# Kernel tuning notes

Hardware: AMD Instinct MI355X
Metric: run time of the kernel (lower is better)

The kernel has to match this reference:

```python
import jax, jax.numpy as jnp
import numpy as np

NUM_HEADS = 64
HEAD_DIM = 64
HIDDEN = 2048
STATE = 128
GROUPS = 1
CONVK = 4
CHUNK = 256
INTER = 2 * HIDDEN                       # expand * hidden_size = 4096
CONV_DIM = INTER + 2 * GROUPS * STATE    # 4352
PROJ = INTER + CONV_DIM + NUM_HEADS      # 8512
EPS = 1e-5


def segment_sum(x):
    # x: (..., T) -> (..., T, T) with out[i,j] = sum_{j<k<=i} x[k], -inf above diag
    T = x.shape[-1]
    xe = jnp.broadcast_to(x[..., None], x.shape + (T,))  # [..., i, j] = x[..., i]
    mask_lo = jnp.tril(jnp.ones((T, T), bool), -1)
    xe = jnp.where(mask_lo, xe, 0.0)
    cs = jnp.cumsum(xe, axis=-2)
    mask = jnp.tril(jnp.ones((T, T), bool), 0)
    return jnp.where(mask, cs, -jnp.inf)


def setup_inputs() -> dict:
    key = jax.random.key(0)
    ks = jax.random.split(key, 8)
    b, l = 2, 2048
    s = 0.02
    return {
        "hidden_states": jax.random.normal(ks[0], (b, l, HIDDEN), jnp.float32),
        "in_proj_w": jax.random.normal(ks[1], (PROJ, HIDDEN), jnp.float32) * s,
        "in_proj_b": jax.random.normal(ks[2], (PROJ,), jnp.float32) * 0.01,
        "conv_w": jax.random.normal(ks[3], (CONV_DIM, CONVK), jnp.float32) * 0.1,  # depthwise kernel (torch weight[:,0,:])
        "dt_bias": jnp.ones((NUM_HEADS,), jnp.float32),
        "A_log": jnp.log(jnp.arange(1, NUM_HEADS + 1, dtype=jnp.float32)),
        "D": jnp.ones((NUM_HEADS,), jnp.float32),
        "norm_w": jnp.ones((INTER,), jnp.float32),
        "out_proj_w": jax.random.normal(ks[4], (HIDDEN, INTER), jnp.float32) * s,
        "out_proj_b": jnp.zeros((HIDDEN,), jnp.float32),
    }


def reference(hidden_states, in_proj_w, in_proj_b, conv_w, dt_bias, A_log, D,
              norm_w, out_proj_w, out_proj_b):
    b, l, _ = hidden_states.shape
    proj = hidden_states @ in_proj_w.T + in_proj_b            # (b,l,PROJ)
    gate, hbc, dt = jnp.split(proj, [INTER, INTER + CONV_DIM], axis=-1)

    # causal depthwise conv1d (padding=K-1, truncated to seq_len) + SiLU
    xp = jnp.pad(hbc, ((0, 0), (CONVK - 1, 0), (0, 0)))
    conv = sum(xp[:, j:j + l, :] * conv_w[:, j] for j in range(CONVK))
    hbc = jax.nn.silu(conv)

    x, B, C = jnp.split(hbc, [INTER, INTER + GROUPS * STATE], axis=-1)
    A = -jnp.exp(A_log)                                       # (h,)
    dt = jax.nn.softplus(dt + dt_bias)                        # (b,l,h)
    dt = jnp.clip(dt, 0.0, None)                              # time_step_limit = (0, inf)

    x = x.reshape(b, l, NUM_HEADS, HEAD_DIM)                  # (b,l,h,p)
    rep = NUM_HEADS // GROUPS
    Bh = jnp.repeat(B.reshape(b, l, GROUPS, STATE), rep, axis=2)  # (b,l,h,n)
    Ch = jnp.repeat(C.reshape(b, l, GROUPS, STATE), rep, axis=2)

    pad = (CHUNK - l % CHUNK) % CHUNK

    def chunk(t):
        t = jnp.pad(t, ((0, 0), (0, pad)) + ((0, 0),) * (t.ndim - 2))
        return t.reshape(b, -1, CHUNK, *t.shape[2:])

    xc = chunk(x * dt[..., None])                             # (b,c,s,h,p) discretized x
    Ac = chunk(A * dt)                                        # (b,c,s,h)
    Bc = chunk(Bh)                                            # (b,c,s,h,n)
    Cc = chunk(Ch)

    Ach = jnp.transpose(Ac, (0, 3, 1, 2))                     # (b,h,c,s)
    A_cumsum = jnp.cumsum(Ach, axis=-1)

    # 1. intra-chunk (diagonal block) outputs
    L = jnp.exp(segment_sum(Ach))                             # (b,h,c,s,s)
    Y_diag = jnp.einsum('bcthn,bcshn,bhcts,bcshp->bcthp', Cc, Bc, L, xc)

    # 2. per-chunk final states
    decay_states = jnp.exp(A_cumsum[..., -1:] - A_cumsum)     # (b,h,c,s)
    states = jnp.einsum('bcshn,bhcs,bcshp->bchpn', Bc, decay_states, xc)

    # 3. inter-chunk recurrence
    A_last = jnp.pad(A_cumsum[..., -1], ((0, 0), (0, 0), (1, 0)))  # (b,h,c+1)
    decay_chunk = jnp.exp(segment_sum(A_last))                # (b,h,c+1,c+1)
    states0 = jnp.concatenate([jnp.zeros_like(states[:, :1]), states], axis=1)
    prev = jnp.einsum('bhzc,bchpn->bzhpn', decay_chunk, states0)[:, :-1]  # (b,c,h,p,n)

    # 4. state -> output contribution
    state_decay_out = jnp.exp(A_cumsum)                       # (b,h,c,s)
    Y_off = jnp.einsum('bcshn,bchpn,bhcs->bcshp', Cc, prev, state_decay_out)

    Y = (Y_diag + Y_off).reshape(b, -1, NUM_HEADS, HEAD_DIM)[:, :l]
    y = Y + D[:, None] * x                                    # D skip connection
    y = y.reshape(b, l, INTER)

    # gated RMSNorm (gate applied before normalization)
    g = y * jax.nn.silu(gate)
    var = jnp.mean(g * g, axis=-1, keepdims=True)
    g = g * jax.lax.rsqrt(var + EPS) * norm_w

    return g @ out_proj_w.T + out_proj_b                      # (b,l,HIDDEN)
```

## Files before the change

### kernel.cpp

```cpp
#include <hip/hip_runtime.h>

typedef __bf16 bf16;
typedef __bf16 bf16x8 __attribute__((ext_vector_type(8)));
typedef __bf16 bf16x4 __attribute__((ext_vector_type(4)));
typedef float  floatx4 __attribute__((ext_vector_type(4)));

#define HIDDEN   2048
#define NUMH     64
#define HDIM     64
#define STATE    128
#define INTER    4096
#define CONV_DIM 4352
#define PROJ_N   8512
#define PROJ_PAD 8576
#define SEQ      2048
#define BATCH    2
#define CHUNK    256
#define NCHUNK   8
#define ROWS     4096
#define DT_COL0  8448

#define GLDS(gp, lp) __builtin_amdgcn_global_load_lds(                      \
    (const __attribute__((address_space(1))) void*)(gp),                    \
    (__attribute__((address_space(3))) void*)(lp), 16, 0, 0)

__global__ __launch_bounds__(256) void cvt_bf16_kernel(
    const float* __restrict__ in, bf16* __restrict__ out, long n, long srcn) {
  long i = ((long)blockIdx.x * 256 + threadIdx.x) * 4;
  if (i >= n) return;
  if (i + 3 < srcn) {
    const float* p = in + i;
    bf16x4 o;
    o[0] = (bf16)p[0]; o[1] = (bf16)p[1]; o[2] = (bf16)p[2]; o[3] = (bf16)p[3];
    *(bf16x4*)(out + i) = o;
  } else {
    for (int j = 0; j < 4; j++) {
      float v = (i + j < srcn) ? in[i + j] : 0.f;
      out[i + j] = (bf16)v;
    }
  }
}

__global__ __launch_bounds__(256, 2) void gemm_bt_kernel(
    const bf16* __restrict__ A, const bf16* __restrict__ B,
    const float* __restrict__ bias, bf16* __restrict__ Cb,
    float* __restrict__ Cf, float* __restrict__ ds,
    int M, int N, int K, int bias_n, int dt0) {
  __shared__ __align__(16) bf16 lA[2 * 128 * 32];
  __shared__ __align__(16) bf16 lB[2 * 128 * 32];
  const int tid  = threadIdx.x;
  const int lane = tid & 63;
  const int wave = tid >> 6;
  const int gm = M >> 7;
  const int id = blockIdx.x;
  const int xcd = id & 7;
  const int j = id >> 3;
  const int mstripe = gm >> 3;
  const int mb = xcd * mstripe + (j % mstripe);
  const int nb = j / mstripe;
  const int m0 = mb * 128;
  const int n0 = nb * 128;
  const int wm = (wave >> 1) * 64;
  const int wn = (wave & 1) * 64;
  const int q  = lane >> 4;
  const int ln = lane & 15;
  const int r0 = tid >> 2;
  const int c0 = (tid & 3) * 8;

  floatx4 acc[4][4] = {};

  const bf16* Ap = A + (long)(m0 + r0) * K + c0;
  const bf16* Bp = B + (long)(n0 + r0) * K + c0;
  bf16* lAw = lA + wave * 512;
  bf16* lBw = lB + wave * 512;

  for (int k0 = 0; k0 < K; k0 += 64) {
    __syncthreads();
    GLDS(Ap + k0, lAw);
    GLDS(Ap + (long)64 * K + k0, lAw + 2048);
    GLDS(Ap + k0 + 32, lAw + 4096);
    GLDS(Ap + (long)64 * K + k0 + 32, lAw + 6144);
    GLDS(Bp + k0, lBw);
    GLDS(Bp + (long)64 * K + k0, lBw + 2048);
    GLDS(Bp + k0 + 32, lBw + 4096);
    GLDS(Bp + (long)64 * K + k0 + 32, lBw + 6144);
    __syncthreads();
#pragma unroll
    for (int kc = 0; kc < 2; kc++) {
      bf16x8 af[4], bg[4];
#pragma unroll
      for (int i = 0; i < 4; i++) {
        af[i] = *(const bf16x8*)(lA + kc * 4096 + (wm + i * 16 + ln) * 32 + q * 8);
        bg[i] = *(const bf16x8*)(lB + kc * 4096 + (wn + i * 16 + ln) * 32 + q * 8);
      }
#pragma unroll
      for (int mi = 0; mi < 4; mi++)
#pragma unroll
        for (int ni = 0; ni < 4; ni++)
          acc[mi][ni] = __builtin_amdgcn_mfma_f32_16x16x32_bf16(
              af[mi], bg[ni], acc[mi][ni], 0, 0, 0);
    }
  }

#pragma unroll
  for (int mi = 0; mi < 4; mi++) {
#pragma unroll
    for (int ni = 0; ni < 4; ni++) {
      int col = n0 + wn + ni * 16 + ln;
      float bv = (col < bias_n) ? bias[col] : 0.f;
#pragma unroll
      for (int r = 0; r < 4; r++) {
        int row = m0 + wm + mi * 16 + q * 4 + r;
        float v = acc[mi][ni][r] + bv;
        if (Cb) Cb[(long)row * N + col] = (bf16)v;
        else    Cf[(long)row * N + col] = v;
        if (ds && col >= dt0 && col < dt0 + 64)
          ds[(long)row * 64 + (col - dt0)] = v;
      }
    }
  }
}

__global__ __launch_bounds__(256) void conv_silu_kernel(
    const bf16* __restrict__ proj, const float* __restrict__ cw,
    bf16* __restrict__ out) {
  long i = ((long)blockIdx.x * 256 + threadIdx.x) * 4;
  if (i >= (long)ROWS * CONV_DIM) return;
  int ch = (int)(i % CONV_DIM);
  long bl = i / CONV_DIM;
  int l = (int)(bl & (SEQ - 1));
  const bf16* p = proj + bl * PROJ_PAD + INTER + ch;
  float a[4] = {0.f, 0.f, 0.f, 0.f};
#pragma unroll
  for (int tap = 0; tap < 4; tap++) {
    int back = 3 - tap;
    if (l >= back) {
      bf16x4 v = *(const bf16x4*)(p - (long)back * PROJ_PAD);
#pragma unroll
      for (int j = 0; j < 4; j++) a[j] += (float)v[j] * cw[(ch + j) * 4 + tap];
    }
  }
  bf16x4 o;
#pragma unroll
  for (int j = 0; j < 4; j++) {
    float s = a[j] / (1.f + expf(-a[j]));
    o[j] = (bf16)s;
  }
  *(bf16x4*)(out + i) = o;
}

__global__ __launch_bounds__(256) void dt_scan_kernel(
    const float* __restrict__ dtraw, const float* __restrict__ dt_bias,
    const float* __restrict__ A_log, float* __restrict__ dtb,
    float* __restrict__ cumA) {
  int idx = blockIdx.x;
  int c = idx & 7, h = (idx >> 3) & 63, b = idx >> 9;
  int s = threadIdx.x;
  long row = (long)b * SEQ + c * CHUNK + s;
  float x = dtraw[row * NUMH + h] + dt_bias[h];
  float dt = (x > 20.f) ? x : log1pf(expf(x));
  dtb[row * NUMH + h] = dt;
  float dA = -expf(A_log[h]) * dt;
  __shared__ float sc[256];
  sc[s] = dA;
  __syncthreads();
  for (int off = 1; off < 256; off <<= 1) {
    float v = (s >= off) ? sc[s - off] : 0.f;
    __syncthreads();
    sc[s] += v;
    __syncthreads();
  }
  cumA[(long)idx * 256 + s] = sc[s];
}

__global__ __launch_bounds__(256, 2) void g_kernel(
    const bf16* __restrict__ conv, float* __restrict__ G) {
  int bc = blockIdx.x, tt = blockIdx.y, sb = blockIdx.z;
  if (sb > tt) return;
  int b = bc >> 3, c = bc & 7;
  int tid = threadIdx.x, lane = tid & 63, w = tid >> 6;
  int q = lane >> 4, ln = lane & 15;
  __shared__ __align__(16) bf16 sCg[4 * 64 * 32];
  __shared__ __align__(16) bf16 sBg[4 * 64 * 32];
  long rowBase = (long)b * SEQ + c * CHUNK;
  for (int i = tid; i < 1024; i += 256) {
    int r = i >> 4, n0 = (i & 15) * 8;
    int base = ((n0 >> 5) * 64 + r) * 32 + (n0 & 31);
    bf16x8 cv = *(const bf16x8*)(conv + (rowBase + tt * 64 + r) * CONV_DIM + INTER + STATE + n0);
    *(bf16x8*)(sCg + base) = cv;
    bf16x8 bv = *(const bf16x8*)(conv + (rowBase + sb * 64 + r) * CONV_DIM + INTER + n0);
    *(bf16x8*)(sBg + base) = bv;
  }
  __syncthreads();
  floatx4 acc[4] = {};
#pragma unroll
  for (int kc = 0; kc < 4; kc++) {
    bf16x8 af = *(const bf16x8*)(sCg + (kc * 64 + w * 16 + ln) * 32 + q * 8);
#pragma unroll
    for (int ni = 0; ni < 4; ni++) {
      bf16x8 bg = *(const bf16x8*)(sBg + (kc * 64 + ni * 16 + ln) * 32 + q * 8);
      acc[ni] = __builtin_amdgcn_mfma_f32_16x16x32_bf16(af, bg, acc[ni], 0, 0, 0);
    }
  }
  float* Gb = G + ((long)bc << 16);
#pragma unroll
  for (int ni = 0; ni < 4; ni++) {
    int s = sb * 64 + ni * 16 + ln;
#pragma unroll
    for (int r = 0; r < 4; r++) {
      int t = tt * 64 + w * 16 + q * 4 + r;
      Gb[(long)t * 256 + s] = acc[ni][r];
    }
  }
}

__global__ __launch_bounds__(256, 2) void states_kernel(
    const bf16* __restrict__ conv, const float* __restrict__ dtb,
    const float* __restrict__ cumA, float* __restrict__ S) {
  int idx = blockIdx.x;
  int h = idx & 63, c = (idx >> 6) & 7, b = idx >> 9;
  int tid = threadIdx.x, lane = tid & 63, w = tid >> 6;
  int q = lane >> 4, ln = lane & 15;
  __shared__ __align__(16) bf16 sBT[2 * 128 * 32];
  __shared__ __align__(16) bf16 sXT[2 * 64 * 32];
  long caBase = ((long)(b * 64 + h) * 8 + c) * 256;
  float aLast = cumA[caBase + 255];
  long rowBase = (long)b * SEQ + c * CHUNK;
  floatx4 acc[2][4] = {};
  for (int s0 = 0; s0 < 256; s0 += 64) {
    __syncthreads();
    for (int i = tid; i < 1024; i += 256) {
      int sl = i >> 4, n0 = (i & 15) * 8;
      bf16x8 v = *(const bf16x8*)(conv + (rowBase + s0 + sl) * CONV_DIM + INTER + n0);
      int base = ((sl >> 5) * 128 + n0) * 32 + (sl & 31);
#pragma unroll
      for (int jj = 0; jj < 8; jj++) sBT[base + jj * 32] = v[jj];
    }
    for (int i = tid; i < 512; i += 256) {
      int sl = i >> 3, p0 = (i & 7) * 8;
      long row = rowBase + s0 + sl;
      float wgt = __expf(aLast - cumA[caBase + s0 + sl]) * dtb[row * NUMH + h];
      bf16x8 v = *(const bf16x8*)(conv + row * CONV_DIM + h * HDIM + p0);
      int base = ((sl >> 5) * 64 + p0) * 32 + (sl & 31);
#pragma unroll
      for (int jj = 0; jj < 8; jj++) sXT[base + jj * 32] = (bf16)((float)v[jj] * wgt);
    }
    __syncthreads();
#pragma unroll
    for (int kc = 0; kc < 2; kc++) {
      bf16x8 af[2], bg[4];
#pragma unroll
      for (int mi = 0; mi < 2; mi++)
        af[mi] = *(const bf16x8*)(sBT + (kc * 128 + w * 32 + mi * 16 + ln) * 32 + q * 8);
#pragma unroll
      for (int ni = 0; ni < 4; ni++)
        bg[ni] = *(const bf16x8*)(sXT + (kc * 64 + ni * 16 + ln) * 32 + q * 8);
#pragma unroll
      for (int mi = 0; mi < 2; mi++)
#pragma unroll
        for (int ni = 0; ni < 4; ni++)
          acc[mi][ni] = __builtin_amdgcn_mfma_f32_16x16x32_bf16(
              af[mi], bg[ni], acc[mi][ni], 0, 0, 0);
    }
  }
  float* Sp = S + ((long)idx << 13);
#pragma unroll
  for (int mi = 0; mi < 2; mi++)
#pragma unroll
    for (int ni = 0; ni < 4; ni++) {
      int p = ni * 16 + ln;
#pragma unroll
      for (int r = 0; r < 4; r++) {
        int n = w * 32 + mi * 16 + q * 4 + r;
        Sp[n * 64 + p] = acc[mi][ni][r];
      }
    }
}

__global__ __launch_bounds__(256) void recur_kernel(
    const float* __restrict__ S, const float* __restrict__ cumA,
    float* __restrict__ P) {
  int bh = blockIdx.x, kq = blockIdx.y;
  int b = bh >> 6, h = bh & 63;
  int tid = threadIdx.x;
  float p[8];
#pragma unroll
  for (int k = 0; k < 8; k++) p[k] = 0.f;
  for (int c = 0; c < 8; c++) {
    long blk = ((long)(b * 8 + c) * 64 + h) << 13;
#pragma unroll
    for (int k = 0; k < 8; k++) P[blk + (kq * 8 + k) * 256 + tid] = p[k];
    float e = __expf(cumA[((long)bh * 8 + c) * 256 + 255]);
#pragma unroll
    for (int k = 0; k < 8; k++) p[k] = S[blk + (kq * 8 + k) * 256 + tid] + e * p[k];
  }
}

__global__ __launch_bounds__(256, 2) void y_kernel(
    const bf16* __restrict__ conv, const float* __restrict__ dtb,
    const float* __restrict__ cumA, const float* __restrict__ G,
    const float* __restrict__ P, const float* __restrict__ D,
    bf16* __restrict__ ybuf) {
  int idx = blockIdx.x;
  int h = idx & 63, c = (idx >> 6) & 7, b = idx >> 9;
  int tid = threadIdx.x, lane = tid & 63, w = tid >> 6;
  int q = lane >> 4, ln = lane & 15;
  __shared__ __align__(16) bf16 sPT[128 * 64];
  __shared__ __align__(16) bf16 sXT[256 * 64];
  __shared__ float scA[256];
  __shared__ float sE[256];
  long caBase = ((long)(b * 64 + h) * 8 + c) * 256;
  long rowBase = (long)b * SEQ + c * CHUNK;
  const float* Gbase = G + ((long)(b * 8 + c) << 16);

  float myA = cumA[caBase + tid];
  scA[tid] = myA;
  {
    const float* Pblk = P + ((long)idx << 13);
    int n = tid >> 1;
    int p0 = (tid & 1) * 32;
    int nc = (n >> 5) * 64, nk = n & 31;
#pragma unroll
    for (int pp = 0; pp < 32; pp += 4) {
      floatx4 v = *(const floatx4*)(Pblk + n * 64 + p0 + pp);
#pragma unroll
      for (int j = 0; j < 4; j++)
        sPT[(nc + p0 + pp + j) * 32 + nk] = (bf16)v[j];
    }
  }
  {
    int s = tid;
    long row = rowBase + s;
    float dt = dtb[row * NUMH + h];
    int sc = (s >> 5) * 64, sk = s & 31;
    const bf16* xr = conv + row * CONV_DIM + h * HDIM;
#pragma unroll
    for (int p0 = 0; p0 < 64; p0 += 8) {
      bf16x8 xv = *(const bf16x8*)(xr + p0);
#pragma unroll
      for (int j = 0; j < 8; j++)
        sXT[(sc + p0 + j) * 32 + sk] = (bf16)((float)xv[j] * dt);
    }
  }
  __syncthreads();
  sE[tid] = __expf(scA[tid | 63] - myA);

  floatx4 acc[4][4] = {};

  const bf16* Cbase = conv + (rowBase + w * 64) * CONV_DIM + INTER + STATE;
  for (int k0 = 0; k0 < 128; k0 += 32) {
    bf16x8 af[4], bg[4];
#pragma unroll
    for (int mi = 0; mi < 4; mi++)
      af[mi] = *(const bf16x8*)(Cbase + (long)(mi * 16 + ln) * CONV_DIM + k0 + q * 8);
#pragma unroll
    for (int ni = 0; ni < 4; ni++)
      bg[ni] = *(const bf16x8*)(sPT + ((k0 >> 5) * 64 + ni * 16 + ln) * 32 + q * 8);
#pragma unroll
    for (int mi = 0; mi < 4; mi++)
#pragma unroll
      for (int ni = 0; ni < 4; ni++)
        acc[mi][ni] = __builtin_amdgcn_mfma_f32_16x16x32_bf16(
            af[mi], bg[ni], acc[mi][ni], 0, 0, 0);
  }
#pragma unroll
  for (int mi = 0; mi < 4; mi++)
#pragma unroll
    for (int r = 0; r < 4; r++) {
      float e = __expf(scA[w * 64 + mi * 16 + q * 4 + r]);
#pragma unroll
      for (int ni = 0; ni < 4; ni++) acc[mi][ni][r] *= e;
    }
  __syncthreads();

  for (int sb = 0; sb < w; sb++) {
    float Rm[4];
#pragma unroll
    for (int mi = 0; mi < 4; mi++)
      Rm[mi] = __expf(scA[w * 64 + mi * 16 + ln] - scA[sb * 64 + 63]);
#pragma unroll
    for (int kk = 0; kk < 64; kk += 32) {
      int s0 = sb * 64 + kk;
      bf16x8 af[4], bg[4];
#pragma unroll
      for (int mi = 0; mi < 4; mi++) {
        int t = w * 64 + mi * 16 + ln;
        const float* Gr = Gbase + (long)t * 256 + s0 + q * 8;
        floatx4 g0 = *(const floatx4*)Gr;
        floatx4 g1 = *(const floatx4*)(Gr + 4);
        bf16x8 m;
#pragma unroll
        for (int j = 0; j < 4; j++)
          m[j] = (bf16)(g0[j] * Rm[mi] * sE[s0 + q * 8 + j]);
#pragma unroll
        for (int j = 4; j < 8; j++)
          m[j] = (bf16)(g1[j - 4] * Rm[mi] * sE[s0 + q * 8 + j]);
        af[mi] = m;
      }
#pragma unroll
      for (int ni = 0; ni < 4; ni++)
        bg[ni] = *(const bf16x8*)(sXT + ((s0 >> 5) * 64 + ni * 16 + ln) * 32 + q * 8);
#pragma unroll
      for (int mi = 0; mi < 4; mi++)
#pragma unroll
        for (int ni = 0; ni < 4; ni++)
          acc[mi][ni] = __builtin_amdgcn_mfma_f32_16x16x32_bf16(
              af[mi], bg[ni], acc[mi][ni], 0, 0, 0);
    }
  }

  {
    int sb = w;
#pragma unroll
    for (int kk = 0; kk < 64; kk += 32) {
      int s0 = sb * 64 + kk;
      bf16x8 af[4], bg[4];
#pragma unroll
      for (int mi = 0; mi < 4; mi++) {
        int t = w * 64 + mi * 16 + ln;
        float cAt = scA[t];
        const float* Gr = Gbase + (long)t * 256 + s0 + q * 8;
        floatx4 g0 = *(const floatx4*)Gr;
        floatx4 g1 = *(const floatx4*)(Gr + 4);
        bf16x8 m;
#pragma unroll
        for (int j = 0; j < 4; j++) {
          int s = s0 + q * 8 + j;
          float v = g0[j] * __expf(cAt - scA[s]);
          m[j] = (bf16)((s <= t) ? v : 0.f);
        }
#pragma unroll
        for (int j = 4; j < 8; j++) {
          int s = s0 + q * 8 + j;
          float v = g1[j - 4] * __expf(cAt - scA[s]);
          m[j] = (bf16)((s <= t) ? v : 0.f);
        }
        af[mi] = m;
      }
#pragma unroll
      for (int ni = 0; ni < 4; ni++)
        bg[ni] = *(const bf16x8*)(sXT + ((s0 >> 5) * 64 + ni * 16 + ln) * 32 + q * 8);
#pragma unroll
      for (int mi = 0; mi < 4; mi++)
#pragma unroll
        for (int ni = 0; ni < 4; ni++)
          acc[mi][ni] = __builtin_amdgcn_mfma_f32_16x16x32_bf16(
              af[mi], bg[ni], acc[mi][ni], 0, 0, 0);
    }
  }

  float d = D[h];
#pragma unroll
  for (int mi = 0; mi < 4; mi++)
#pragma unroll
    for (int ni = 0; ni < 4; ni++) {
      int col = ni * 16 + ln;
#pragma unroll
      for (int r = 0; r < 4; r++) {
        long row = rowBase + w * 64 + mi * 16 + q * 4 + r;
        float xv = (float)conv[row * CONV_DIM + h * HDIM + col];
        ybuf[row * INTER + h * HDIM + col] = (bf16)(acc[mi][ni][r] + d * xv);
      }
    }
}

__global__ __launch_bounds__(256) void rmsnorm_kernel(
    const bf16* __restrict__ ybuf, const bf16* __restrict__ proj,
    const float* __restrict__ nw, bf16* __restrict__ gb) {
  long row = blockIdx.x;
  int tid = threadIdx.x;
  float gv[16];
  float ss = 0.f;
#pragma unroll
  for (int k = 0; k < 16; k++) {
    int i = k * 256 + tid;
    float y = (float)ybuf[row * INTER + i];
    float gt = (float)proj[row * PROJ_PAD + i];
    float g = y * (gt / (1.f + expf(-gt)));
    gv[k] = g;
    ss += g * g;
  }
#pragma unroll
  for (int off = 32; off > 0; off >>= 1) ss += __shfl_down(ss, off, 64);
  __shared__ float red[4];
  if ((tid & 63) == 0) red[tid >> 6] = ss;
  __syncthreads();
  float tot = red[0] + red[1] + red[2] + red[3];
  float scale = rsqrtf(tot * (1.f / 4096.f) + 1e-5f);
#pragma unroll
  for (int k = 0; k < 16; k++) {
    int i = k * 256 + tid;
    gb[row * INTER + i] = (bf16)(gv[k] * scale * nw[i]);
  }
}

extern "C" void kernel_launch(void* const* d_in, const int* in_sizes, int n_in,
                              void* d_out, int out_size, void* d_ws, size_t ws_size,
                              hipStream_t stream) {
  const float* hs   = (const float*)d_in[0];
  const float* ipw  = (const float*)d_in[1];
  const float* ipb  = (const float*)d_in[2];
  const float* cw   = (const float*)d_in[3];
  const float* dtbi = (const float*)d_in[4];
  const float* alog = (const float*)d_in[5];
  const float* Dp   = (const float*)d_in[6];
  const float* nw   = (const float*)d_in[7];
  const float* opw  = (const float*)d_in[8];
  const float* opb  = (const float*)d_in[9];
  float* out = (float*)d_out;

  char* ws = (char*)d_ws;
  bf16*  hsb   = (bf16*)(ws + 0);
  bf16*  wb    = (bf16*)(ws + 16777216);
  float* S     = (float*)(ws + 0);
  bf16*  ybuf  = (bf16*)(ws + 0);
  bf16*  owb   = (bf16*)(ws + 35127296);
  bf16*  proj  = (bf16*)(ws + 51904512);
  bf16*  conv  = (bf16*)(ws + 122159104);
  float* dtraw = (float*)(ws + 157810688);
  float* dtb   = (float*)(ws + 158859264);
  float* cumA  = (float*)(ws + 159907840);
  float* G     = (float*)(ws + 160956416);
  float* P     = (float*)(ws + 165150720);
  bf16*  gb    = (bf16*)(ws + 165150720);

  cvt_bf16_kernel<<<8192, 256, 0, stream>>>(hs, hsb, (long)ROWS * HIDDEN, (long)ROWS * HIDDEN);
  cvt_bf16_kernel<<<17152, 256, 0, stream>>>(ipw, wb, (long)PROJ_PAD * HIDDEN, (long)PROJ_N * HIDDEN);

  gemm_bt_kernel<<<(PROJ_PAD / 128) * (ROWS / 128), 256, 0, stream>>>(
      hsb, wb, ipb, proj, nullptr, dtraw, ROWS, PROJ_PAD, HIDDEN, PROJ_N, DT_COL0);

  cvt_bf16_kernel<<<8192, 256, 0, stream>>>(opw, owb, (long)HIDDEN * INTER, (long)HIDDEN * INTER);

  conv_silu_kernel<<<17408, 256, 0, stream>>>(proj, cw, conv);

  dt_scan_kernel<<<1024, 256, 0, stream>>>(dtraw, dtbi, alog, dtb, cumA);

  g_kernel<<<dim3(16, 4, 4), 256, 0, stream>>>(conv, G);

  states_kernel<<<1024, 256, 0, stream>>>(conv, dtb, cumA, S);

  recur_kernel<<<dim3(128, 4), 256, 0, stream>>>(S, cumA, P);

  y_kernel<<<1024, 256, 0, stream>>>(conv, dtb, cumA, G, P, Dp, ybuf);

  rmsnorm_kernel<<<4096, 256, 0, stream>>>(ybuf, proj, nw, gb);

  gemm_bt_kernel<<<(HIDDEN / 128) * (ROWS / 128), 256, 0, stream>>>(
      gb, owb, opb, nullptr, out, nullptr, ROWS, HIDDEN, INTER, HIDDEN, 1 << 30);
}
```

Baseline: 662.0 us.

## Use 256x256-tile double-buffered GEMM kernel for input projection

Adds a new 512-thread GEMM kernel with 256x256 output tiles, swizzled LDS, direct global-to-LDS loads, double buffering and MFMA scheduling hints, and uses it for the input projection. The projection width is padded to 8704 so it divides by 256, and the workspace offsets are shifted to match. Larger tiles raise arithmetic intensity and cut redundant global loads, but padding adds wasted columns and fewer, bigger blocks may hurt occupancy or tail balance.

```diff
diff --git a/kernel.cpp b/kernel.cpp
--- a/kernel.cpp
+++ b/kernel.cpp
@@ -12,7 +12,7 @@
 #define INTER    4096
 #define CONV_DIM 4352
 #define PROJ_N   8512
-#define PROJ_PAD 8576
+#define PROJ_PAD 8704
 #define SEQ      2048
 #define BATCH    2
 #define CHUNK    256
@@ -37,6 +37,127 @@
     for (int j = 0; j < 4; j++) {
       float v = (i + j < srcn) ? in[i + j] : 0.f;
       out[i + j] = (bf16)v;
+    }
+  }
+}
+
+__global__ __launch_bounds__(512, 4) void gemm256_kernel(
+    const bf16* __restrict__ A, const bf16* __restrict__ B,
+    const float* __restrict__ bias, bf16* __restrict__ Cb,
+    float* __restrict__ ds,
+    int M, int N, int K, int bias_n, int dt0) {
+  __shared__ __align__(16) bf16 lA0[256 * 32], lA1[256 * 32];
+  __shared__ __align__(16) bf16 lB0[256 * 32], lB1[256 * 32];
+  const int tid  = threadIdx.x;
+  const int lane = tid & 63;
+  const int wave = tid >> 6;
+  const int wm   = wave >> 2;
+  const int wn   = wave & 3;
+  const int q    = lane >> 4;
+  const int ln   = lane & 15;
+
+  const int mtiles  = M >> 8;
+  const int mstripe = mtiles >> 3;
+  const int id  = blockIdx.x;
+  const int xcd = id & 7;
+  const int jj  = id >> 3;
+  const int mb  = xcd * mstripe + (jj % mstripe);
+  const int nb  = jj / mstripe;
+  const int m0  = mb << 8;
+  const int n0  = nb << 8;
+
+  const int rA0 = tid >> 2;
+  const int rA1 = 128 + (tid >> 2);
+  const int cc  = tid & 3;
+  const int qa0 = cc ^ ((rA0 >> 1) & 3);
+  const int qa1 = cc ^ ((rA1 >> 1) & 3);
+  const bf16* srcA0 = A + (long)(m0 + rA0) * K + qa0 * 8;
+  const bf16* srcA1 = A + (long)(m0 + rA1) * K + qa1 * 8;
+  const bf16* srcB0 = B + (long)(n0 + rA0) * K + qa0 * 8;
+  const bf16* srcB1 = B + (long)(n0 + rA1) * K + qa1 * 8;
+
+  int aoff[8], boff[4];
+#pragma unroll
+  for (int mi = 0; mi < 8; mi++) {
+    int ra = wm * 128 + mi * 16 + ln;
+    aoff[mi] = ra * 32 + ((q ^ ((ra >> 1) & 3)) * 8);
+  }
+#pragma unroll
+  for (int ni = 0; ni < 4; ni++) {
+    int rb = wn * 64 + ni * 16 + ln;
+    boff[ni] = rb * 32 + ((q ^ ((rb >> 1) & 3)) * 8);
+  }
+
+  floatx4 acc[8][4] = {};
+
+  auto phase = [&](const bf16* aS, const bf16* bS, bf16* aD, bf16* bD,
+                   int kn, bool doStage) {
+    if (doStage) {
+      GLDS(srcA0 + kn, aD + wave * 512);
+      GLDS(srcA1 + kn, aD + 4096 + wave * 512);
+      GLDS(srcB0 + kn, bD + wave * 512);
+      GLDS(srcB1 + kn, bD + 4096 + wave * 512);
+    }
+    __builtin_amdgcn_sched_barrier(0);
+    bf16x8 af[8], bg[4];
+#pragma unroll
+    for (int mi = 0; mi < 4; mi++) af[mi] = *(const bf16x8*)(aS + aoff[mi]);
+#pragma unroll
+    for (int ni = 0; ni < 4; ni++) bg[ni] = *(const bf16x8*)(bS + boff[ni]);
+    __builtin_amdgcn_sched_barrier(0);
+#pragma unroll
+    for (int mi = 4; mi < 8; mi++) af[mi] = *(const bf16x8*)(aS + aoff[mi]);
+    asm volatile("s_waitcnt lgkmcnt(4)" ::: "memory");
+    __builtin_amdgcn_sched_barrier(0);
+    __builtin_amdgcn_s_setprio(1);
+#pragma unroll
+    for (int mi = 0; mi < 4; mi++)
+#pragma unroll
+      for (int ni = 0; ni < 4; ni++)
+        acc[mi][ni] = __builtin_amdgcn_mfma_f32_16x16x32_bf16(
+            af[mi], bg[ni], acc[mi][ni], 0, 0, 0);
+    __builtin_amdgcn_s_setprio(0);
+    asm volatile("s_waitcnt lgkmcnt(0)" ::: "memory");
+    __builtin_amdgcn_sched_barrier(0);
+    __builtin_amdgcn_s_setprio(1);
+#pragma unroll
+    for (int mi = 4; mi < 8; mi++)
+#pragma unroll
+      for (int ni = 0; ni < 4; ni++)
+        acc[mi][ni] = __builtin_amdgcn_mfma_f32_16x16x32_bf16(
+            af[mi], bg[ni], acc[mi][ni], 0, 0, 0);
+    __builtin_amdgcn_s_setprio(0);
+    asm volatile("s_waitcnt vmcnt(0)" ::: "memory");
+    __builtin_amdgcn_s_barrier();
+  };
+
+  GLDS(srcA0, lA0 + wave * 512);
+  GLDS(srcA1, lA0 + 4096 + wave * 512);
+  GLDS(srcB0, lB0 + wave * 512);
+  GLDS(srcB1, lB0 + 4096 + wave * 512);
+  asm volatile("s_waitcnt vmcnt(0)" ::: "memory");
+  __builtin_amdgcn_s_barrier();
+
+  const int NC = K >> 5;
+  for (int j = 0; j < NC; j += 2) {
+    phase(lA0, lB0, lA1, lB1, (j + 1) << 5, true);
+    phase(lA1, lB1, lA0, lB0, (j + 2) << 5, (j + 2) < NC);
+  }
+
+#pragma unroll
+  for (int mi = 0; mi < 8; mi++) {
+#pragma unroll
+    for (int ni = 0; ni < 4; ni++) {
+      int col = n0 + wn * 64 + ni * 16 + ln;
+      float bv = (col < bias_n) ? bias[col] : 0.f;
+#pragma unroll
+      for (int r = 0; r < 4; r++) {
+        int row = m0 + wm * 128 + mi * 16 + q * 4 + r;
+        float v = acc[mi][ni][r] + bv;
+        Cb[(long)row * N + col] = (bf16)v;
+        if (ds && col >= dt0 && col < dt0 + 64)
+          ds[(long)row * 64 + (col - dt0)] = v;
+      }
     }
   }
 }
@@ -515,20 +636,20 @@
   float* S     = (float*)(ws + 0);
   bf16*  ybuf  = (bf16*)(ws + 0);
   bf16*  owb   = (bf16*)(ws + 35127296);
-  bf16*  proj  = (bf16*)(ws + 51904512);
-  bf16*  conv  = (bf16*)(ws + 122159104);
-  float* dtraw = (float*)(ws + 157810688);
-  float* dtb   = (float*)(ws + 158859264);
-  float* cumA  = (float*)(ws + 159907840);
-  float* G     = (float*)(ws + 160956416);
-  float* P     = (float*)(ws + 165150720);
-  bf16*  gb    = (bf16*)(ws + 165150720);
+  bf16*  proj  = (bf16*)(ws + 52428800);
+  bf16*  conv  = (bf16*)(ws + 123731968);
+  float* dtraw = (float*)(ws + 159383552);
+  float* dtb   = (float*)(ws + 160432128);
+  float* cumA  = (float*)(ws + 161480704);
+  float* G     = (float*)(ws + 162529280);
+  float* P     = (float*)(ws + 166723584);
+  bf16*  gb    = (bf16*)(ws + 166723584);
 
   cvt_bf16_kernel<<<8192, 256, 0, stream>>>(hs, hsb, (long)ROWS * HIDDEN, (long)ROWS * HIDDEN);
-  cvt_bf16_kernel<<<17152, 256, 0, stream>>>(ipw, wb, (long)PROJ_PAD * HIDDEN, (long)PROJ_N * HIDDEN);
-
-  gemm_bt_kernel<<<(PROJ_PAD / 128) * (ROWS / 128), 256, 0, stream>>>(
-      hsb, wb, ipb, proj, nullptr, dtraw, ROWS, PROJ_PAD, HIDDEN, PROJ_N, DT_COL0);
+  cvt_bf16_kernel<<<17408, 256, 0, stream>>>(ipw, wb, (long)PROJ_PAD * HIDDEN, (long)PROJ_N * HIDDEN);
+
+  gemm256_kernel<<<(ROWS / 256) * (PROJ_PAD / 256), 512, 0, stream>>>(
+      hsb, wb, ipb, proj, dtraw, ROWS, PROJ_PAD, HIDDEN, PROJ_N, DT_COL0);
 
   cvt_bf16_kernel<<<8192, 256, 0, stream>>>(opw, owb, (long)HIDDEN * INTER, (long)HIDDEN * INTER);
 
```

Result: slower. 2.309 ms (+248.8%).

## Triple-buffer GEMM LDS tiles with swizzled layout and overlapped global loads

Applied to the files above, without the earlier changes.

Replaces the single-buffer, two-barrier-per-step GEMM mainloop with a three-stage LDS ring over K-steps of 32. The next tile is issued via global_load_lds while the current one is computed, with vmcnt-based waits and one barrier per step. It also XOR-swizzles the LDS column chunks to cut bank conflicts, and raises the MFMA priority during compute. Occupancy hint goes from 2 to 3 blocks per CU, which may raise register pressure, and there is more synchronization per unit of K.

```diff
diff --git a/kernel.cpp b/kernel.cpp
--- a/kernel.cpp
+++ b/kernel.cpp
@@ -41,13 +41,12 @@
   }
 }
 
-__global__ __launch_bounds__(256, 2) void gemm_bt_kernel(
+__global__ __launch_bounds__(256, 3) void gemm_bt_kernel(
     const bf16* __restrict__ A, const bf16* __restrict__ B,
     const float* __restrict__ bias, bf16* __restrict__ Cb,
     float* __restrict__ Cf, float* __restrict__ ds,
     int M, int N, int K, int bias_n, int dt0) {
-  __shared__ __align__(16) bf16 lA[2 * 128 * 32];
-  __shared__ __align__(16) bf16 lB[2 * 128 * 32];
+  __shared__ __align__(16) bf16 lds[3 * 8192];
   const int tid  = threadIdx.x;
   const int lane = tid & 63;
   const int wave = tid >> 6;
@@ -65,42 +64,82 @@
   const int q  = lane >> 4;
   const int ln = lane & 15;
   const int r0 = tid >> 2;
-  const int c0 = (tid & 3) * 8;
+  const int c0 = tid & 3;
+  const int qa = c0 ^ ((r0 >> 1) & 3);
+
+  const bf16* srcA = A + (long)(m0 + r0) * K + qa * 8;
+  const bf16* srcB = B + (long)(n0 + r0) * K + qa * 8;
+  const long rs64 = (long)64 * K;
+
+  int aoff[4], boff[4];
+#pragma unroll
+  for (int i = 0; i < 4; i++) {
+    int ra = wm + i * 16 + ln;
+    aoff[i] = ra * 32 + ((q ^ ((ra >> 1) & 3)) * 8);
+    int rb = wn + i * 16 + ln;
+    boff[i] = rb * 32 + ((q ^ ((rb >> 1) & 3)) * 8) + 4096;
+  }
 
   floatx4 acc[4][4] = {};
 
-  const bf16* Ap = A + (long)(m0 + r0) * K + c0;
-  const bf16* Bp = B + (long)(n0 + r0) * K + c0;
-  bf16* lAw = lA + wave * 512;
-  bf16* lBw = lB + wave * 512;
-
-  for (int k0 = 0; k0 < K; k0 += 64) {
-    __syncthreads();
-    GLDS(Ap + k0, lAw);
-    GLDS(Ap + (long)64 * K + k0, lAw + 2048);
-    GLDS(Ap + k0 + 32, lAw + 4096);
-    GLDS(Ap + (long)64 * K + k0 + 32, lAw + 6144);
-    GLDS(Bp + k0, lBw);
-    GLDS(Bp + (long)64 * K + k0, lBw + 2048);
-    GLDS(Bp + k0 + 32, lBw + 4096);
-    GLDS(Bp + (long)64 * K + k0 + 32, lBw + 6144);
-    __syncthreads();
-#pragma unroll
-    for (int kc = 0; kc < 2; kc++) {
-      bf16x8 af[4], bg[4];
-#pragma unroll
-      for (int i = 0; i < 4; i++) {
-        af[i] = *(const bf16x8*)(lA + kc * 4096 + (wm + i * 16 + ln) * 32 + q * 8);
-        bg[i] = *(const bf16x8*)(lB + kc * 4096 + (wn + i * 16 + ln) * 32 + q * 8);
-      }
-#pragma unroll
-      for (int mi = 0; mi < 4; mi++)
-#pragma unroll
-        for (int ni = 0; ni < 4; ni++)
-          acc[mi][ni] = __builtin_amdgcn_mfma_f32_16x16x32_bf16(
-              af[mi], bg[ni], acc[mi][ni], 0, 0, 0);
-    }
-  }
+#define STAGE(gA, gB, so)                                                   \
+  do {                                                                      \
+    bf16* dA = lds + (so) + wave * 512;                                     \
+    bf16* dB = lds + (so) + 4096 + wave * 512;                              \
+    GLDS((gA), dA);                                                         \
+    GLDS((gA) + rs64, dA + 2048);                                           \
+    GLDS((gB), dB);                                                         \
+    GLDS((gB) + rs64, dB + 2048);                                           \
+  } while (0)
+
+#define COMPUTE(so)                                                         \
+  do {                                                                      \
+    bf16x8 af[4], bg[4];                                                    \
+    _Pragma("unroll")                                                       \
+    for (int i = 0; i < 4; i++) {                                           \
+      af[i] = *(const bf16x8*)(lds + (so) + aoff[i]);                       \
+      bg[i] = *(const bf16x8*)(lds + (so) + boff[i]);                       \
+    }                                                                       \
+    asm volatile("s_waitcnt lgkmcnt(0)" ::: "memory");                      \
+    __builtin_amdgcn_sched_barrier(0);                                      \
+    __builtin_amdgcn_s_setprio(1);                                          \
+    _Pragma("unroll")                                                       \
+    for (int mi = 0; mi < 4; mi++)                                          \
+      _Pragma("unroll")                                                     \
+      for (int ni = 0; ni < 4; ni++)                                        \
+        acc[mi][ni] = __builtin_amdgcn_mfma_f32_16x16x32_bf16(              \
+            af[mi], bg[ni], acc[mi][ni], 0, 0, 0);                          \
+    __builtin_amdgcn_s_setprio(0);                                          \
+  } while (0)
+
+  const int NC = K >> 5;
+  int s0 = 0, s1 = 8192, s2 = 16384;
+
+  STAGE(srcA, srcB, s0);
+  STAGE(srcA + 32, srcB + 32, s1);
+  asm volatile("s_waitcnt vmcnt(4)" ::: "memory");
+  __builtin_amdgcn_s_barrier();
+  __builtin_amdgcn_sched_barrier(0);
+
+  const bf16* gA = srcA + 64;
+  const bf16* gB = srcB + 64;
+  for (int p = 0; p < NC - 2; ++p) {
+    STAGE(gA, gB, s2);
+    gA += 32; gB += 32;
+    COMPUTE(s0);
+    asm volatile("s_waitcnt vmcnt(4)" ::: "memory");
+    __builtin_amdgcn_s_barrier();
+    __builtin_amdgcn_sched_barrier(0);
+    int t = s0; s0 = s1; s1 = s2; s2 = t;
+  }
+  COMPUTE(s0);
+  asm volatile("s_waitcnt vmcnt(0)" ::: "memory");
+  __builtin_amdgcn_s_barrier();
+  __builtin_amdgcn_sched_barrier(0);
+  COMPUTE(s1);
+
+#undef STAGE
+#undef COMPUTE
 
 #pragma unroll
   for (int mi = 0; mi < 4; mi++) {
```

New measurement: 679.9 us. +2.7%, slower.

## Use 256x256-tile double-buffered MFMA GEMM for input projection

Applied to the files above, without the earlier changes.

Replaces the 128x128 tiled in-projection GEMM with a new 512-thread kernel that computes 256x256 output tiles. It uses direct global-to-LDS loads with XOR swizzling, double-buffered 64-wide K stages, and interleaved barriers with priority hints. Projection padding rises to 8704 so N divides by 256, and workspace offsets shift to fit. Larger tiles cut global and LDS traffic per FLOP, at the cost of a fuller LDS, heavier register use, padded wasted columns and fewer blocks.

```diff
diff --git a/kernel.cpp b/kernel.cpp
--- a/kernel.cpp
+++ b/kernel.cpp
@@ -12,7 +12,7 @@
 #define INTER    4096
 #define CONV_DIM 4352
 #define PROJ_N   8512
-#define PROJ_PAD 8576
+#define PROJ_PAD 8704
 #define SEQ      2048
 #define BATCH    2
 #define CHUNK    256
@@ -37,6 +37,138 @@
     for (int j = 0; j < 4; j++) {
       float v = (i + j < srcn) ? in[i + j] : 0.f;
       out[i + j] = (bf16)v;
+    }
+  }
+}
+
+__global__ __launch_bounds__(512, 2) void gemm256_kernel(
+    const bf16* __restrict__ A, const bf16* __restrict__ B,
+    const float* __restrict__ bias, bf16* __restrict__ Cb,
+    float* __restrict__ ds, int M, int N, int K, int bias_n, int dt0) {
+  __shared__ __align__(16) bf16 lds[2 * 32768];
+  const int tid  = threadIdx.x;
+  const int lane = tid & 63;
+  const int w    = tid >> 6;
+  const int wm   = w >> 2;
+  const int wn   = w & 3;
+  const int q    = lane >> 4;
+  const int ln   = lane & 15;
+
+  const int mtiles  = M >> 8;
+  const int mstripe = mtiles >> 3;
+  const int id  = blockIdx.x;
+  const int xcd = id & 7;
+  const int jj  = id >> 3;
+  const int m0  = (xcd * mstripe + (jj % mstripe)) << 8;
+  const int n0  = (jj / mstripe) << 8;
+
+  const int w512 = w * 512;
+  const bf16* pA = A + (long)(m0 + w * 8 + (lane >> 3)) * K
+                     + ((lane & 7) ^ ((lane >> 3) & 7)) * 8;
+  const bf16* pB = B + (long)(n0 + w * 8 + (lane >> 3)) * K
+                     + ((lane & 7) ^ ((lane >> 3) & 7)) * 8;
+
+  const int chk0 = ((0 + q) ^ (ln & 7)) * 8;
+  const int chk1 = ((4 + q) ^ (ln & 7)) * 8;
+  const int abase = wm * 8192 + ln * 64;
+  const int bbase = 16384 + wn * 4096 + ln * 64;
+
+  floatx4 acc[8][4] = {};
+  bf16x8 bg0, bg1, bg2, bg3;
+
+#define SG2(sp, kt, o1, ro1, o2, ro2)                                       \
+  do { const bf16* g_ = (sp) + (long)(kt) * 64;                             \
+    GLDS(g_ + (long)(ro1) * K, lds + (o1) + w512);                          \
+    GLDS(g_ + (long)(ro2) * K, lds + (o2) + w512); } while (0)
+
+#define S_AX(kt, be) SG2(pA, kt, (be) + 0,      0,  (be) + 8192, 128)
+#define S_AY(kt, be) SG2(pA, kt, (be) + 4096,  64,  (be) + 12288, 192)
+#define S_B0(kt, be) SG2(pB, kt, (be) + 16384,  0,  (be) + 20480, 64)
+#define S_B1(kt, be) SG2(pB, kt, (be) + 24576, 128, (be) + 28672, 192)
+
+#define MM(AF, MI)                                                          \
+  acc[MI][0] = __builtin_amdgcn_mfma_f32_16x16x32_bf16(AF, bg0, acc[MI][0], 0, 0, 0); \
+  acc[MI][1] = __builtin_amdgcn_mfma_f32_16x16x32_bf16(AF, bg1, acc[MI][1], 0, 0, 0); \
+  acc[MI][2] = __builtin_amdgcn_mfma_f32_16x16x32_bf16(AF, bg2, acc[MI][2], 0, 0, 0); \
+  acc[MI][3] = __builtin_amdgcn_mfma_f32_16x16x32_bf16(AF, bg3, acc[MI][3], 0, 0, 0)
+
+#define VM4 asm volatile("s_waitcnt vmcnt(4)" ::: "memory")
+#define VM0 asm volatile("s_waitcnt vmcnt(0)" ::: "memory")
+
+#define PH(be, CHK, MH, RDBG, STMT, VM)                                     \
+  {                                                                         \
+    const bf16* ap_ = lds + (be) + abase + (CHK) + (MH) * 4096;             \
+    bf16x8 a0_ = *(const bf16x8*)(ap_);                                     \
+    bf16x8 a1_ = *(const bf16x8*)(ap_ + 1024);                              \
+    bf16x8 a2_ = *(const bf16x8*)(ap_ + 2048);                              \
+    bf16x8 a3_ = *(const bf16x8*)(ap_ + 3072);                              \
+    if (RDBG) {                                                             \
+      const bf16x8* bp_ = (const bf16x8*)(lds + (be) + bbase + (CHK));      \
+      bg0 = bp_[0]; bg1 = bp_[128]; bg2 = bp_[256]; bg3 = bp_[384];         \
+    }                                                                       \
+    STMT;                                                                   \
+    __builtin_amdgcn_s_barrier();                                           \
+    asm volatile("s_waitcnt lgkmcnt(0)" ::: "memory");                      \
+    __builtin_amdgcn_sched_barrier(0);                                      \
+    __builtin_amdgcn_s_setprio(1);                                          \
+    MM(a0_, (MH) * 4 + 0); MM(a1_, (MH) * 4 + 1);                           \
+    MM(a2_, (MH) * 4 + 2); MM(a3_, (MH) * 4 + 3);                           \
+    __builtin_amdgcn_s_setprio(0);                                          \
+    VM;                                                                     \
+    __builtin_amdgcn_s_barrier();                                           \
+  }
+
+  S_AX(0, 0); S_AY(0, 0); S_B0(0, 0); S_B1(0, 0);
+  S_AX(1, 32768); S_B0(1, 32768);
+  VM4;
+  __builtin_amdgcn_s_barrier();
+
+  const int NI = K >> 7;
+  for (int i = 0; i < NI - 1; ++i) {
+    const int k1 = 2 * i + 1, k2 = 2 * i + 2, k3 = 2 * i + 3;
+    PH(0,     chk0, 0, 1, { S_AY(k1, 32768); S_B1(k1, 32768); }, (void)0);
+    PH(0,     chk0, 1, 0, (void)0, (void)0);
+    PH(0,     chk1, 0, 1, (void)0, (void)0);
+    PH(0,     chk1, 1, 0, { S_AX(k2, 0); S_B0(k2, 0); }, VM4);
+    PH(32768, chk0, 0, 1, { S_AY(k2, 0); S_B1(k2, 0); }, (void)0);
+    PH(32768, chk0, 1, 0, (void)0, (void)0);
+    PH(32768, chk1, 0, 1, (void)0, (void)0);
+    PH(32768, chk1, 1, 0, { S_AX(k3, 32768); S_B0(k3, 32768); }, VM4);
+  }
+  {
+    const int k1 = (K >> 6) - 1;
+    PH(0,     chk0, 0, 1, { S_AY(k1, 32768); S_B1(k1, 32768); }, (void)0);
+    PH(0,     chk0, 1, 0, (void)0, (void)0);
+    PH(0,     chk1, 0, 1, (void)0, (void)0);
+    PH(0,     chk1, 1, 0, (void)0, VM0);
+    PH(32768, chk0, 0, 1, (void)0, (void)0);
+    PH(32768, chk0, 1, 0, (void)0, (void)0);
+    PH(32768, chk1, 0, 1, (void)0, (void)0);
+    PH(32768, chk1, 1, 0, (void)0, (void)0);
+  }
+
+#undef PH
+#undef MM
+#undef S_AX
+#undef S_AY
+#undef S_B0
+#undef S_B1
+#undef SG2
+
+#pragma unroll
+  for (int mi = 0; mi < 8; mi++) {
+#pragma unroll
+    for (int ni = 0; ni < 4; ni++) {
+      int col = n0 + wn * 64 + ni * 16 + ln;
+      float bv = (col < bias_n) ? bias[col] : 0.f;
+#pragma unroll
+      for (int r = 0; r < 4; r++) {
+        int row = m0 + wm * 128 + mi * 16 + q * 4 + r;
+        float v = acc[mi][ni][r] + bv;
+        Cb[(long)row * N + col] = (bf16)v;
+        if (col >= dt0 && col < dt0 + 64)
+          ds[(long)row * 64 + (col - dt0)] = v;
+      }
     }
   }
 }
@@ -515,20 +647,20 @@
   float* S     = (float*)(ws + 0);
   bf16*  ybuf  = (bf16*)(ws + 0);
   bf16*  owb   = (bf16*)(ws + 35127296);
-  bf16*  proj  = (bf16*)(ws + 51904512);
-  bf16*  conv  = (bf16*)(ws + 122159104);
-  float* dtraw = (float*)(ws + 157810688);
-  float* dtb   = (float*)(ws + 158859264);
-  float* cumA  = (float*)(ws + 159907840);
-  float* G     = (float*)(ws + 160956416);
-  float* P     = (float*)(ws + 165150720);
-  bf16*  gb    = (bf16*)(ws + 165150720);
+  bf16*  proj  = (bf16*)(ws + 52428800);
+  bf16*  conv  = (bf16*)(ws + 123731968);
+  float* dtraw = (float*)(ws + 159383552);
+  float* dtb   = (float*)(ws + 160432128);
+  float* cumA  = (float*)(ws + 161480704);
+  float* G     = (float*)(ws + 162529280);
+  float* P     = (float*)(ws + 166723584);
+  bf16*  gb    = (bf16*)(ws + 166723584);
 
   cvt_bf16_kernel<<<8192, 256, 0, stream>>>(hs, hsb, (long)ROWS * HIDDEN, (long)ROWS * HIDDEN);
-  cvt_bf16_kernel<<<17152, 256, 0, stream>>>(ipw, wb, (long)PROJ_PAD * HIDDEN, (long)PROJ_N * HIDDEN);
-
-  gemm_bt_kernel<<<(PROJ_PAD / 128) * (ROWS / 128), 256, 0, stream>>>(
-      hsb, wb, ipb, proj, nullptr, dtraw, ROWS, PROJ_PAD, HIDDEN, PROJ_N, DT_COL0);
+  cvt_bf16_kernel<<<17408, 256, 0, stream>>>(ipw, wb, (long)PROJ_PAD * HIDDEN, (long)PROJ_N * HIDDEN);
+
+  gemm256_kernel<<<(ROWS / 256) * (PROJ_PAD / 256), 512, 0, stream>>>(
+      hsb, wb, ipb, proj, dtraw, ROWS, PROJ_PAD, HIDDEN, PROJ_N, DT_COL0);
 
   cvt_bf16_kernel<<<8192, 256, 0, stream>>>(opw, owb, (long)HIDDEN * INTER, (long)HIDDEN * INTER);
 
```

New measurement: 689.1 us. +4.1%, slower.
